# Kernel tuning notes

Measured on AMD Instinct MI355X. Metric: run time of the kernel, lower is better.

Reference implementation:

```python
import jax, jax.numpy as jnp
import numpy as np

EPS = 1e-12


def setup_inputs() -> dict:
    key = jax.random.key(0)
    k1, k2, k3, k4 = jax.random.split(key, 4)
    N, H, W, D, K = 64, 32, 32, 512, 64
    x = jax.random.normal(k1, (N, H, W, D), dtype=jnp.float32)
    W_assign = jax.random.normal(k2, (D, K), dtype=jnp.float32) * 0.05  # 1x1 conv kernel
    b_assign = jax.random.normal(k3, (K,), dtype=jnp.float32) * 0.05
    C = jax.random.normal(k4, (D, K), dtype=jnp.float32) * 0.05  # cluster centers
    return {"x": x, "W_assign": W_assign, "b_assign": b_assign, "C": C}


def _l2norm(v, axis):
    return v / jnp.sqrt(jnp.sum(v * v, axis=axis, keepdims=True) + EPS)


def reference(x, W_assign, b_assign, C):
    # 1x1 conv = matmul over channel dim: [N,H,W,D] @ [D,K] -> [N,H,W,K]
    s = jnp.einsum('nhwd,dk->nhwk', x, W_assign) + b_assign
    a = jax.nn.softmax(s, axis=-1)                       # soft assignment over K
    # VLAD: v[n,d,k] = sum_hw a[n,h,w,k] * (x[n,h,w,d] + C[d,k])
    # reformulated as two small contractions (no [N,H,W,D,K] intermediate):
    v = jnp.einsum('nhwd,nhwk->ndk', x, a)               # feature-weighted sums
    a_sum = jnp.sum(a, axis=(1, 2))                      # [N,K]
    v = v + a_sum[:, None, :] * C[None, :, :]            # [N,D,K]
    # intra-normalization: L2 over D per cluster (after transpose to [N,K,D])
    v = _l2norm(jnp.transpose(v, (0, 2, 1)), axis=-1)    # [N,K,D]
    v = jnp.transpose(v, (0, 2, 1))                      # [N,D,K]
    # flatten and final L2 normalize -> [N, D*K]
    v = v.reshape(v.shape[0], -1)
    return _l2norm(v, axis=-1)
```

## Files before the change

### kernel.cpp

```cpp
#include <hip/hip_runtime.h>


#define EPSF 1e-12f

typedef short bf16x8 __attribute__((ext_vector_type(8)));
typedef float f32x16 __attribute__((ext_vector_type(16)));

__device__ inline unsigned short f2bf_rne(float f) {
  union { float f; unsigned u; } v; v.f = f;
  unsigned u = v.u;
  unsigned r = u + 0x7fffu + ((u >> 16) & 1u);
  return (unsigned short)(r >> 16);
}
__device__ inline unsigned pk2(float a, float b) {
#if __has_builtin(__builtin_amdgcn_cvt_pk_bf16_f32)
  auto r = __builtin_amdgcn_cvt_pk_bf16_f32(a, b);
  return __builtin_bit_cast(unsigned, r);
#else
  return (unsigned)f2bf_rne(a) | ((unsigned)f2bf_rne(b) << 16);
#endif
}

__global__ __launch_bounds__(256) void kprep(
    const float* __restrict__ Wm, unsigned short* __restrict__ wt,
    float* __restrict__ stats ) {
  const int t = threadIdx.x, bx = blockIdx.x;
  if (bx == 8) {
    float4 z = {0.f, 0.f, 0.f, 0.f};
#pragma unroll
    for (int r = 0; r < 8; ++r)
      *(float4*)&stats[(size_t)(r * 256 + t) * 4] = z;
    return;
  }
  __shared__ float tile[64][65];
  {
    int col = (t & 15) * 4, rbase = t >> 4;
#pragma unroll
    for (int r = 0; r < 4; ++r) {
      int row = rbase + 16 * r;
      *(float4*)&tile[row][col] =
          *(const float4*)&Wm[(size_t)(bx * 64 + row) * 64 + col];
    }
  }
  __syncthreads();
  int k = t >> 2, seg = (t & 3) * 16;
  size_t o = (size_t)k * 512 + bx * 64 + seg;
#pragma unroll
  for (int j = 0; j < 16; j += 2)
    *(unsigned*)&wt[o + j] = pk2(tile[seg + j][k], tile[seg + j + 1][k]);
}

__global__ __launch_bounds__(256, 1) void kfused(
    const float* __restrict__ x, const unsigned short* __restrict__ wt,
    const float* __restrict__ b, float* __restrict__ vpart,
    float* __restrict__ a_sum) {
  __shared__ unsigned short xbT[512 * 128];
  __shared__ unsigned short ab[64 * 128];
  const int t = threadIdx.x;
  const int w = t >> 6, lane = t & 63, l31 = lane & 31, h = lane >> 5;
  const int bid = blockIdx.x;
  const int n = bid >> 2, c = bid & 3;
  const unsigned short* w0 = wt + (size_t)l31 * 512;
  const unsigned short* w1 = wt + (size_t)(32 + l31) * 512;
  const float bias0 = b[l31], bias1 = b[32 + l31];
  const int colpx = w * 32 + l31;

  f32x16 accv[8];
#pragma unroll
  for (int i = 0; i < 8; ++i)
#pragma unroll
    for (int j = 0; j < 16; ++j) accv[i][j] = 0.f;

  float asum0 = 0.f, asum1 = 0.f;

  for (int s = 0; s < 2; ++s) {
    const int pxb = c * 256 + s * 128;
    const float* rowp = x + ((size_t)n * 1024 + pxb + colpx) * 512;
    f32x16 s0, s1;
#pragma unroll
    for (int i = 0; i < 16; ++i) { s0[i] = 0.f; s1[i] = 0.f; }
#pragma unroll 8
    for (int st = 0; st < 32; ++st) {
      const int kd = st * 16 + h * 8;
      float4 xa = *(const float4*)&rowp[kd];
      float4 xb = *(const float4*)&rowp[kd + 4];
      union { unsigned u[4]; bf16x8 v; } ax;
      ax.u[0] = pk2(xa.x, xa.y);
      ax.u[1] = pk2(xa.z, xa.w);
      ax.u[2] = pk2(xb.x, xb.y);
      ax.u[3] = pk2(xb.z, xb.w);
      bf16x8 b0 = *(const bf16x8*)&w0[kd];
      bf16x8 b1 = *(const bf16x8*)&w1[kd];
      s0 = __builtin_amdgcn_mfma_f32_32x32x16_bf16(ax.v, b0, s0, 0, 0, 0);
      s1 = __builtin_amdgcn_mfma_f32_32x32x16_bf16(ax.v, b1, s1, 0, 0, 0);
#pragma unroll
      for (int j2 = 0; j2 < 4; ++j2) {
        const int da = kd + 2 * j2, db = da + 1;
        xbT[da * 128 + (colpx ^ ((da & 15) << 3))] =
            (unsigned short)(ax.u[j2] & 0xffffu);
        xbT[db * 128 + (colpx ^ ((db & 15) << 3))] =
            (unsigned short)(ax.u[j2] >> 16);
      }
    }
    float a0[16], a1[16];
    float sum0 = 0.f, sum1 = 0.f;
#pragma unroll
    for (int r = 0; r < 16; ++r) {
      float v0 = s0[r] + bias0, v1 = s1[r] + bias1;
      float m = fmaxf(v0, v1);
#pragma unroll
      for (int msk = 1; msk < 32; msk <<= 1)
        m = fmaxf(m, __shfl_xor(m, msk, 64));
      float e0 = __expf(v0 - m), e1 = __expf(v1 - m);
      float S = e0 + e1;
#pragma unroll
      for (int msk = 1; msk < 32; msk <<= 1) S += __shfl_xor(S, msk, 64);
      float inv = 1.0f / S;
      a0[r] = e0 * inv; a1[r] = e1 * inv;
      sum0 += a0[r]; sum1 += a1[r];
    }
    asum0 += sum0; asum1 += sum1;
#pragma unroll
    for (int g = 0; g < 4; ++g) {
      const int cb = w * 32 + 8 * g + 4 * h;
      uint2 uu;
      uu.x = pk2(a0[4 * g + 0], a0[4 * g + 1]);
      uu.y = pk2(a0[4 * g + 2], a0[4 * g + 3]);
      *(uint2*)&ab[l31 * 128 + (cb ^ ((l31 & 15) << 3))] = uu;
      uu.x = pk2(a1[4 * g + 0], a1[4 * g + 1]);
      uu.y = pk2(a1[4 * g + 2], a1[4 * g + 3]);
      *(uint2*)&ab[(32 + l31) * 128 + (cb ^ ((l31 & 15) << 3))] = uu;
    }
    __syncthreads();
    const int dw = w * 128;
#pragma unroll
    for (int s8 = 0; s8 < 8; ++s8) {
      const int px0 = s8 * 16 + 8 * h;
      bf16x8 bb0 = *(const bf16x8*)&ab[l31 * 128 + (px0 ^ ((l31 & 15) << 3))];
      bf16x8 bb1 =
          *(const bf16x8*)&ab[(32 + l31) * 128 + (px0 ^ ((l31 & 15) << 3))];
#pragma unroll
      for (int dt = 0; dt < 4; ++dt) {
        const int dr = dw + dt * 32 + l31;
        bf16x8 aa = *(const bf16x8*)&xbT[dr * 128 + (px0 ^ ((dr & 15) << 3))];
        accv[dt * 2 + 0] =
            __builtin_amdgcn_mfma_f32_32x32x16_bf16(aa, bb0, accv[dt * 2 + 0], 0, 0, 0);
        accv[dt * 2 + 1] =
            __builtin_amdgcn_mfma_f32_32x32x16_bf16(aa, bb1, accv[dt * 2 + 1], 0, 0, 0);
      }
    }
    __syncthreads();
  }
  asum0 += __shfl_xor(asum0, 32, 64);
  asum1 += __shfl_xor(asum1, 32, 64);
  if (lane < 32) {
    atomicAdd(&a_sum[n * 64 + l31], asum0);
    atomicAdd(&a_sum[n * 64 + 32 + l31], asum1);
  }
  float* vp = vpart + (size_t)c * 2097152 + (size_t)n * 32768;
#pragma unroll
  for (int dt = 0; dt < 4; ++dt) {
#pragma unroll
    for (int kt = 0; kt < 2; ++kt) {
      const f32x16 a = accv[dt * 2 + kt];
      const int kcol = kt * 32 + l31;
#pragma unroll
      for (int r = 0; r < 16; ++r) {
        const int drow = w * 128 + dt * 32 + (r & 3) + 8 * (r >> 2) + 4 * h;
        vp[drow * 64 + kcol] = a[r];
      }
    }
  }
}

__global__ __launch_bounds__(256) void kpost(
    const float* __restrict__ vpart, const float* __restrict__ a_sum,
    const float* __restrict__ C, float* __restrict__ out,
    float* __restrict__ ssq) {
  const int bid = blockIdx.x;
  const int n = bid & 63, d0 = (bid >> 6) * 64;
  const int t = threadIdx.x, k = t & 63, dr = t >> 6;
  const float as = a_sum[n * 64 + k];
  const size_t nb = (size_t)n * 32768;
  float sq = 0.f;
#pragma unroll
  for (int r = 0; r < 16; ++r) {
    const int d = d0 + dr * 16 + r;
    const size_t idx = nb + (size_t)d * 64 + k;
    float o = vpart[idx] + vpart[idx + 2097152] + vpart[idx + 4194304] +
              vpart[idx + 6291456] + as * C[(size_t)d * 64 + k];
    out[idx] = o;
    sq += o * o;
  }
  atomicAdd(&ssq[n * 64 + k], sq);
}

__global__ __launch_bounds__(256) void kscale(
    float* __restrict__ out, const float* __restrict__ ssq) {
  const int n = blockIdx.y, slice = blockIdx.x;
  const int t = threadIdx.x, k = t & 63, rg = t >> 6;
  __shared__ float sk[64];
  __shared__ float tot;
  if (t < 64) {
    float cc = ssq[n * 64 + t];
    sk[t] = rsqrtf(cc + EPSF);
    float contrib = cc / (cc + EPSF);
#pragma unroll
    for (int m = 32; m; m >>= 1) contrib += __shfl_xor(contrib, m, 64);
    if (t == 0) tot = rsqrtf(contrib + EPSF);
  }
  __syncthreads();
  const float scale = sk[k] * tot;
  float* vb = out + (size_t)n * 32768 + (size_t)slice * 4096;
#pragma unroll
  for (int r = rg; r < 64; r += 4) vb[r * 64 + k] *= scale;
}

extern "C" void kernel_launch(void* const* d_in, const int* in_sizes, int n_in,
                              void* d_out, int out_size, void* d_ws, size_t ws_size,
                              hipStream_t stream) {
  const float* x  = (const float*)d_in[0];
  const float* Wm = (const float*)d_in[1];
  const float* b  = (const float*)d_in[2];
  const float* C  = (const float*)d_in[3];
  float* out = (float*)d_out;

  float* vpart = (float*)d_ws;
  unsigned short* wt = (unsigned short*)(vpart + 4 * 2097152);
  float* stats = (float*)(wt + (size_t)64 * 512);
  float* a_sum = stats;
  float* ssq   = stats + 4096;

  kprep<<<dim3(9), dim3(256), 0, stream>>>(Wm, wt, stats);
  kfused<<<dim3(256), dim3(256), 0, stream>>>(x, wt, b, vpart, a_sum);
  kpost<<<dim3(512), dim3(256), 0, stream>>>(vpart, a_sum, C, out, ssq);
  kscale<<<dim3(8, 64), dim3(256), 0, stream>>>(out, ssq);
}
```

Measured before the change: 231.3 us.

## Split fused kernel into 512 blocks with specialized assignment and transpose warps

The fused kernel now processes 64-pixel chunks per step over 512 blocks, with half the LDS, and requests two blocks per CU. Warps 0-1 compute the assignment GEMM and softmax while warps 2-3 load x, convert it to bf16 and write the transposed tile into LDS, where before every warp did both. This aims to raise occupancy and use more CUs on the memory-bound x read. In exchange, x is read twice (once by each warp group), the partial-sum buffer doubles to 8 slices, and kpost has more partials to reduce.

Result: slower. 254.5 us (+10.0%).

```diff
diff --git a/kernel.cpp b/kernel.cpp
--- a/kernel.cpp
+++ b/kernel.cpp
@@ -50,20 +50,21 @@
     *(unsigned*)&wt[o + j] = pk2(tile[seg + j][k], tile[seg + j + 1][k]);
 }
 
-__global__ __launch_bounds__(256, 1) void kfused(
+__global__ __launch_bounds__(256, 2) void kfused(
     const float* __restrict__ x, const unsigned short* __restrict__ wt,
     const float* __restrict__ b, float* __restrict__ vpart,
     float* __restrict__ a_sum) {
-  __shared__ unsigned short xbT[512 * 128];
-  __shared__ unsigned short ab[64 * 128];
+  __shared__ unsigned short xbT[512 * 64];
+  __shared__ unsigned short ab[64 * 64];
   const int t = threadIdx.x;
   const int w = t >> 6, lane = t & 63, l31 = lane & 31, h = lane >> 5;
   const int bid = blockIdx.x;
-  const int n = bid >> 2, c = bid & 3;
+  const int n = bid >> 3, c = bid & 7;
   const unsigned short* w0 = wt + (size_t)l31 * 512;
   const unsigned short* w1 = wt + (size_t)(32 + l31) * 512;
   const float bias0 = b[l31], bias1 = b[32 + l31];
-  const int colpx = w * 32 + l31;
+  const bool gw = (w < 2);
+  const int pxl = (w & 1) * 32 + l31;
 
   f32x16 accv[8];
 #pragma unroll
@@ -74,75 +75,89 @@
   float asum0 = 0.f, asum1 = 0.f;
 
   for (int s = 0; s < 2; ++s) {
-    const int pxb = c * 256 + s * 128;
-    const float* rowp = x + ((size_t)n * 1024 + pxb + colpx) * 512;
-    f32x16 s0, s1;
-#pragma unroll
-    for (int i = 0; i < 16; ++i) { s0[i] = 0.f; s1[i] = 0.f; }
+    const int pxb = c * 128 + s * 64;
+    const float* rowp = x + ((size_t)n * 1024 + pxb + pxl) * 512;
+    if (gw) {
+      f32x16 s0, s1;
+#pragma unroll
+      for (int i = 0; i < 16; ++i) { s0[i] = 0.f; s1[i] = 0.f; }
 #pragma unroll 8
-    for (int st = 0; st < 32; ++st) {
-      const int kd = st * 16 + h * 8;
-      float4 xa = *(const float4*)&rowp[kd];
-      float4 xb = *(const float4*)&rowp[kd + 4];
-      union { unsigned u[4]; bf16x8 v; } ax;
-      ax.u[0] = pk2(xa.x, xa.y);
-      ax.u[1] = pk2(xa.z, xa.w);
-      ax.u[2] = pk2(xb.x, xb.y);
-      ax.u[3] = pk2(xb.z, xb.w);
-      bf16x8 b0 = *(const bf16x8*)&w0[kd];
-      bf16x8 b1 = *(const bf16x8*)&w1[kd];
-      s0 = __builtin_amdgcn_mfma_f32_32x32x16_bf16(ax.v, b0, s0, 0, 0, 0);
-      s1 = __builtin_amdgcn_mfma_f32_32x32x16_bf16(ax.v, b1, s1, 0, 0, 0);
-#pragma unroll
-      for (int j2 = 0; j2 < 4; ++j2) {
-        const int da = kd + 2 * j2, db = da + 1;
-        xbT[da * 128 + (colpx ^ ((da & 15) << 3))] =
-            (unsigned short)(ax.u[j2] & 0xffffu);
-        xbT[db * 128 + (colpx ^ ((db & 15) << 3))] =
-            (unsigned short)(ax.u[j2] >> 16);
-      }
-    }
-    float a0[16], a1[16];
-    float sum0 = 0.f, sum1 = 0.f;
-#pragma unroll
-    for (int r = 0; r < 16; ++r) {
-      float v0 = s0[r] + bias0, v1 = s1[r] + bias1;
-      float m = fmaxf(v0, v1);
-#pragma unroll
-      for (int msk = 1; msk < 32; msk <<= 1)
-        m = fmaxf(m, __shfl_xor(m, msk, 64));
-      float e0 = __expf(v0 - m), e1 = __expf(v1 - m);
-      float S = e0 + e1;
-#pragma unroll
-      for (int msk = 1; msk < 32; msk <<= 1) S += __shfl_xor(S, msk, 64);
-      float inv = 1.0f / S;
-      a0[r] = e0 * inv; a1[r] = e1 * inv;
-      sum0 += a0[r]; sum1 += a1[r];
-    }
-    asum0 += sum0; asum1 += sum1;
-#pragma unroll
-    for (int g = 0; g < 4; ++g) {
-      const int cb = w * 32 + 8 * g + 4 * h;
-      uint2 uu;
-      uu.x = pk2(a0[4 * g + 0], a0[4 * g + 1]);
-      uu.y = pk2(a0[4 * g + 2], a0[4 * g + 3]);
-      *(uint2*)&ab[l31 * 128 + (cb ^ ((l31 & 15) << 3))] = uu;
-      uu.x = pk2(a1[4 * g + 0], a1[4 * g + 1]);
-      uu.y = pk2(a1[4 * g + 2], a1[4 * g + 3]);
-      *(uint2*)&ab[(32 + l31) * 128 + (cb ^ ((l31 & 15) << 3))] = uu;
+      for (int st = 0; st < 32; ++st) {
+        const int kd = st * 16 + h * 8;
+        float4 xa = *(const float4*)&rowp[kd];
+        float4 xb = *(const float4*)&rowp[kd + 4];
+        union { unsigned u[4]; bf16x8 v; } ax;
+        ax.u[0] = pk2(xa.x, xa.y);
+        ax.u[1] = pk2(xa.z, xa.w);
+        ax.u[2] = pk2(xb.x, xb.y);
+        ax.u[3] = pk2(xb.z, xb.w);
+        bf16x8 b0 = *(const bf16x8*)&w0[kd];
+        bf16x8 b1 = *(const bf16x8*)&w1[kd];
+        s0 = __builtin_amdgcn_mfma_f32_32x32x16_bf16(ax.v, b0, s0, 0, 0, 0);
+        s1 = __builtin_amdgcn_mfma_f32_32x32x16_bf16(ax.v, b1, s1, 0, 0, 0);
+      }
+      float a0[16], a1[16];
+      float sum0 = 0.f, sum1 = 0.f;
+#pragma unroll
+      for (int r = 0; r < 16; ++r) {
+        float v0 = s0[r] + bias0, v1 = s1[r] + bias1;
+        float m = fmaxf(v0, v1);
+#pragma unroll
+        for (int msk = 1; msk < 32; msk <<= 1)
+          m = fmaxf(m, __shfl_xor(m, msk, 64));
+        float e0 = __expf(v0 - m), e1 = __expf(v1 - m);
+        float S = e0 + e1;
+#pragma unroll
+        for (int msk = 1; msk < 32; msk <<= 1) S += __shfl_xor(S, msk, 64);
+        float inv = 1.0f / S;
+        a0[r] = e0 * inv; a1[r] = e1 * inv;
+        sum0 += a0[r]; sum1 += a1[r];
+      }
+      asum0 += sum0; asum1 += sum1;
+#pragma unroll
+      for (int g = 0; g < 4; ++g) {
+        const int cb = (w & 1) * 32 + 8 * g + 4 * h;
+        uint2 uu;
+        uu.x = pk2(a0[4 * g + 0], a0[4 * g + 1]);
+        uu.y = pk2(a0[4 * g + 2], a0[4 * g + 3]);
+        *(uint2*)&ab[l31 * 64 + (cb ^ ((l31 & 7) << 3))] = uu;
+        uu.x = pk2(a1[4 * g + 0], a1[4 * g + 1]);
+        uu.y = pk2(a1[4 * g + 2], a1[4 * g + 3]);
+        *(uint2*)&ab[(32 + l31) * 64 + (cb ^ ((l31 & 7) << 3))] = uu;
+      }
+    } else {
+#pragma unroll 8
+      for (int st = 0; st < 32; ++st) {
+        const int kd = st * 16 + h * 8;
+        float4 xa = *(const float4*)&rowp[kd];
+        float4 xb = *(const float4*)&rowp[kd + 4];
+        unsigned u[4];
+        u[0] = pk2(xa.x, xa.y);
+        u[1] = pk2(xa.z, xa.w);
+        u[2] = pk2(xb.x, xb.y);
+        u[3] = pk2(xb.z, xb.w);
+#pragma unroll
+        for (int j2 = 0; j2 < 4; ++j2) {
+          const int da = kd + 2 * j2, db = da + 1;
+          xbT[da * 64 + (pxl ^ ((da & 7) << 3))] =
+              (unsigned short)(u[j2] & 0xffffu);
+          xbT[db * 64 + (pxl ^ ((db & 7) << 3))] =
+              (unsigned short)(u[j2] >> 16);
+        }
+      }
     }
     __syncthreads();
     const int dw = w * 128;
 #pragma unroll
-    for (int s8 = 0; s8 < 8; ++s8) {
+    for (int s8 = 0; s8 < 4; ++s8) {
       const int px0 = s8 * 16 + 8 * h;
-      bf16x8 bb0 = *(const bf16x8*)&ab[l31 * 128 + (px0 ^ ((l31 & 15) << 3))];
+      bf16x8 bb0 = *(const bf16x8*)&ab[l31 * 64 + (px0 ^ ((l31 & 7) << 3))];
       bf16x8 bb1 =
-          *(const bf16x8*)&ab[(32 + l31) * 128 + (px0 ^ ((l31 & 15) << 3))];
+          *(const bf16x8*)&ab[(32 + l31) * 64 + (px0 ^ ((l31 & 7) << 3))];
 #pragma unroll
       for (int dt = 0; dt < 4; ++dt) {
         const int dr = dw + dt * 32 + l31;
-        bf16x8 aa = *(const bf16x8*)&xbT[dr * 128 + (px0 ^ ((dr & 15) << 3))];
+        bf16x8 aa = *(const bf16x8*)&xbT[dr * 64 + (px0 ^ ((dr & 7) << 3))];
         accv[dt * 2 + 0] =
             __builtin_amdgcn_mfma_f32_32x32x16_bf16(aa, bb0, accv[dt * 2 + 0], 0, 0, 0);
         accv[dt * 2 + 1] =
@@ -151,11 +166,13 @@
     }
     __syncthreads();
   }
-  asum0 += __shfl_xor(asum0, 32, 64);
-  asum1 += __shfl_xor(asum1, 32, 64);
-  if (lane < 32) {
-    atomicAdd(&a_sum[n * 64 + l31], asum0);
-    atomicAdd(&a_sum[n * 64 + 32 + l31], asum1);
+  if (gw) {
+    asum0 += __shfl_xor(asum0, 32, 64);
+    asum1 += __shfl_xor(asum1, 32, 64);
+    if (lane < 32) {
+      atomicAdd(&a_sum[n * 64 + l31], asum0);
+      atomicAdd(&a_sum[n * 64 + 32 + l31], asum1);
+    }
   }
   float* vp = vpart + (size_t)c * 2097152 + (size_t)n * 32768;
 #pragma unroll
@@ -187,8 +204,9 @@
   for (int r = 0; r < 16; ++r) {
     const int d = d0 + dr * 16 + r;
     const size_t idx = nb + (size_t)d * 64 + k;
-    float o = vpart[idx] + vpart[idx + 2097152] + vpart[idx + 4194304] +
-              vpart[idx + 6291456] + as * C[(size_t)d * 64 + k];
+    float o = as * C[(size_t)d * 64 + k];
+#pragma unroll
+    for (int cc = 0; cc < 8; ++cc) o += vpart[idx + (size_t)cc * 2097152];
     out[idx] = o;
     sq += o * o;
   }
@@ -226,13 +244,13 @@
   float* out = (float*)d_out;
 
   float* vpart = (float*)d_ws;
-  unsigned short* wt = (unsigned short*)(vpart + 4 * 2097152);
+  unsigned short* wt = (unsigned short*)(vpart + (size_t)8 * 2097152);
   float* stats = (float*)(wt + (size_t)64 * 512);
   float* a_sum = stats;
   float* ssq   = stats + 4096;
 
   kprep<<<dim3(9), dim3(256), 0, stream>>>(Wm, wt, stats);
-  kfused<<<dim3(256), dim3(256), 0, stream>>>(x, wt, b, vpart, a_sum);
+  kfused<<<dim3(512), dim3(256), 0, stream>>>(x, wt, b, vpart, a_sum);
   kpost<<<dim3(512), dim3(256), 0, stream>>>(vpart, a_sum, C, out, ssq);
   kscale<<<dim3(8, 64), dim3(256), 0, stream>>>(out, ssq);
 }
```
